# Kernel optimization log

Measured on AMD Instinct MI355X. Metric: run time of the kernel, lower is better.

The kernel has to match this reference:

```python
import jax, jax.numpy as jnp
import numpy as np

NP, NA, D, E, C, L = 100000, 50000, 128, 500000, 16, 2


def setup_inputs() -> dict:
    key = jax.random.key(0)
    ks = jax.random.split(key, 16)
    s = 1.0 / np.sqrt(D)
    ei_cites = jnp.stack([jax.random.randint(ks[2], (E,), 0, NP),
                          jax.random.randint(ks[3], (E,), 0, NP)])
    ei_writes = jnp.stack([jax.random.randint(ks[4], (E,), 0, NA),
                           jax.random.randint(ks[5], (E,), 0, NP)])
    ei_rev = jnp.stack([jax.random.randint(ks[6], (E,), 0, NP),
                        jax.random.randint(ks[7], (E,), 0, NA)])
    return {
        'x_paper': jax.random.normal(ks[0], (NP, D), jnp.float32),
        'x_author': jax.random.normal(ks[1], (NA, D), jnp.float32),
        'ei_cites': ei_cites, 'ei_writes': ei_writes, 'ei_rev': ei_rev,
        'Wl': jax.random.normal(ks[8], (L, 3, D, D), jnp.float32) * s,
        'Wr': jax.random.normal(ks[9], (L, 3, D, D), jnp.float32) * s,
        'bl': jnp.zeros((L, 3, D), jnp.float32),
        'lin_paper': jax.random.normal(ks[10], (D, D), jnp.float32) * s,
        'lin_author': jax.random.normal(ks[11], (D, D), jnp.float32) * s,
        'ln_scale': jnp.ones((L, 2, D), jnp.float32),
        'ln_bias': jnp.zeros((L, 2, D), jnp.float32),
        'Wh': jax.random.normal(ks[12], (D, C), jnp.float32) * s,
        'bh': jnp.zeros((C,), jnp.float32),
    }


def _sage(x_src, x_dst, ei, W_l, W_r, b, n_dst):
    # SAGEConv with mean aggregation: lin_l(mean_agg(x_src)) + lin_r(x_dst)
    msg = x_src[ei[0]]                                            # [E, D] gather
    ssum = jax.ops.segment_sum(msg, ei[1], num_segments=n_dst)    # [Ndst, D] scatter
    cnt = jax.ops.segment_sum(jnp.ones((ei.shape[1],), x_src.dtype), ei[1],
                              num_segments=n_dst)
    mean = ssum / jnp.maximum(cnt, 1.0)[:, None]
    return mean @ W_l.T + b + x_dst @ W_r.T


def _ln(x, g, b):
    m = jnp.mean(x, axis=-1, keepdims=True)
    v = jnp.mean(jnp.square(x - m), axis=-1, keepdims=True)
    return (x - m) * jax.lax.rsqrt(v + 1e-5) * g + b


def reference(x_paper, x_author, ei_cites, ei_writes, ei_rev,
              Wl, Wr, bl, lin_paper, lin_author, ln_scale, ln_bias, Wh, bh):
    x_p, x_a = x_paper, x_author
    n_p, n_a = x_p.shape[0], x_a.shape[0]
    for l in range(L):
        # HeteroConv: sum SAGEConv outputs per destination node type
        p_new = (_sage(x_p, x_p, ei_cites, Wl[l, 0], Wr[l, 0], bl[l, 0], n_p)
                 + _sage(x_a, x_p, ei_writes, Wl[l, 1], Wr[l, 1], bl[l, 1], n_p))
        a_new = _sage(x_p, x_a, ei_rev, Wl[l, 2], Wr[l, 2], bl[l, 2], n_a)
        if l < L - 1:  # per-type residual linear (use_linear)
            p_new = p_new + p_new @ lin_paper.T
            a_new = a_new + a_new @ lin_author.T
        x_p = jax.nn.relu(_ln(p_new, ln_scale[l, 0], ln_bias[l, 0]))
        x_a = jax.nn.relu(_ln(a_new, ln_scale[l, 1], ln_bias[l, 1]))
    # head on target node type ('paper')
    return x_p @ Wh + bh
```

## Files before the change

### kernel.cpp

```cpp
#include <hip/hip_runtime.h>
#include <math.h>

#define NPAPER 100000
#define NAUTH  50000
#define DIM    128
#define NEDGE  500000
#define NCLS   16
#define NTOT   (2*NPAPER + NAUTH)
#define NB     245
#define CHUNK_A 11776
#define NBLK_A  128
#define PBLK   ((NPAPER + 127) / 128)
#define ABLK   ((NAUTH  + 127) / 128)

typedef unsigned int   uint;
typedef unsigned short ushort;
typedef unsigned char  uchar;
using short8 = __attribute__((ext_vector_type(8))) short;
using f32x4  = __attribute__((ext_vector_type(4))) float;

__device__ __forceinline__ float b2f(uint u) {
    return __uint_as_float(u << 16);
}
__device__ __forceinline__ ushort f2b(float f) {
    uint x = __float_as_uint(f);
    return (ushort)((x + 0x7fffu + ((x >> 16) & 1u)) >> 16);
}

#define GLD_LDS16(srcp, ldsp) \
    __builtin_amdgcn_global_load_lds( \
        (const __attribute__((address_space(1))) void*)(srcp), \
        (__attribute__((address_space(3))) void*)(ldsp), 16, 0, 0)

__device__ __forceinline__ void prep_weights_body(int b, int tid,
    const float* __restrict__ Wl, const float* __restrict__ Wr,
    const float* __restrict__ bl,
    float* __restrict__ Bp, float* __restrict__ Ba,
    float* __restrict__ biasp, float* __restrict__ biasa)
{
    int t = b * 256 + tid;
    if (t < 2*384*128) {
        int l = t / (384*128); int rem = t - l*(384*128);
        int k = rem >> 7, j = rem & 127;
        float v;
        if (k < 128)      v = Wl[((l*3+0)*128 + j)*128 + k];
        else if (k < 256) v = Wl[((l*3+1)*128 + j)*128 + (k-128)];
        else              v = Wr[((l*3+0)*128 + j)*128 + (k-256)]
                            + Wr[((l*3+1)*128 + j)*128 + (k-256)];
        Bp[t] = v;
        return;
    }
    t -= 2*384*128;
    if (t < 2*256*128) {
        int l = t / (256*128); int rem = t - l*(256*128);
        int k = rem >> 7, j = rem & 127;
        Ba[t] = (k < 128) ? Wl[((l*3+2)*128 + j)*128 + k]
                          : Wr[((l*3+2)*128 + j)*128 + (k-128)];
        return;
    }
    t -= 2*256*128;
    if (t < 256) { int l=t>>7, j=t&127; biasp[t] = bl[(l*3+0)*128+j] + bl[(l*3+1)*128+j]; return; }
    t -= 256;
    if (t < 256) { int l=t>>7, j=t&127; biasa[t] = bl[(l*3+2)*128+j]; return; }
}

__device__ __forceinline__ size_t pack_off(int j, int k) {
    int kstep = k >> 6, ks = (k >> 5) & 1, g4 = (k >> 3) & 3, jj = k & 7;
    int f = j >> 4, l15 = j & 15;
    return (size_t)kstep*8192 + (size_t)(ks*512 + f*64 + g4*16 + l15)*8 + jj;
}

__device__ __forceinline__ void build_bt_body(int b, int tid,
    const float* __restrict__ Bp, const float* __restrict__ Ba,
    const float* __restrict__ linp, const float* __restrict__ lina,
    ushort* __restrict__ Btp, ushort* __restrict__ Bta)
{
    int t = b * 256 + tid;
    if (t < 2*128*384) {
        int l = t / (128*384); int rem = t - l*(128*384);
        int j = rem / 384, k = rem - j*384;
        const float* brow = Bp + (size_t)l*384*128 + (size_t)k*128;
        float v = brow[j];
        if (l == 0) {
            const float* lrow = linp + (size_t)j*128;
            float s = 0.f;
            #pragma unroll 8
            for (int m = 0; m < 128; m++) s += brow[m] * lrow[m];
            v += s;
        }
        Btp[(size_t)l*49152 + pack_off(j, k)] = f2b(v);
        return;
    }
    t -= 2*128*384;
    if (t < 2*128*256) {
        int l = t / (128*256); int rem = t - l*(128*256);
        int j = rem / 256, k = rem - j*256;
        const float* brow = Ba + (size_t)l*256*128 + (size_t)k*128;
        float v = brow[j];
        if (l == 0) {
            const float* lrow = lina + (size_t)j*128;
            float s = 0.f;
            #pragma unroll 8
            for (int m = 0; m < 128; m++) s += brow[m] * lrow[m];
            v += s;
        }
        Bta[(size_t)l*32768 + pack_off(j, k)] = f2b(v);
    }
}

__device__ __forceinline__ void fold_bias_body(int b, int tid,
    const float* __restrict__ biasp, const float* __restrict__ biasa,
    const float* __restrict__ linp, const float* __restrict__ lina,
    float* __restrict__ biasp2, float* __restrict__ biasa2)
{
    int t = b * 256 + tid;
    int isa = t >> 8; int r = t & 255;
    int l = r >> 7, j = r & 127;
    const float* bsrc = isa ? biasa : biasp;
    const float* lin  = isa ? lina  : linp;
    float v = bsrc[r];
    if (l == 0) {
        float s = 0.f;
        for (int k = 0; k < 128; k++) s += bsrc[k] * lin[j*128 + k];
        v += s;
    }
    (isa ? biasa2 : biasp2)[r] = v;
}

__device__ __forceinline__ void to_bf16_body(int b, int tid,
    const float* __restrict__ xp, const float* __restrict__ xa,
    ushort* __restrict__ yp, ushort* __restrict__ ya)
{
    int i = b * 256 + tid;
    const int n4p = NPAPER * DIM / 4;
    const float* x; ushort* y;
    if (i < n4p) { x = xp; y = yp; }
    else { x = xa; y = ya; i -= n4p; }
    float4 v = ((const float4*)x)[i];
    uint2 o;
    o.x = (uint)f2b(v.x) | ((uint)f2b(v.y) << 16);
    o.y = (uint)f2b(v.z) | ((uint)f2b(v.w) << 16);
    ((uint2*)y)[i] = o;
}

__device__ __forceinline__ int edge_g(const int* __restrict__ eiC,
                                      const int* __restrict__ eiW,
                                      const int* __restrict__ eiR, int i)
{
    int tpe = (i >= 2*NEDGE) ? 2 : ((i >= NEDGE) ? 1 : 0);
    int e = i - tpe*NEDGE;
    const int* ei = (tpe == 0) ? eiC : ((tpe == 1) ? eiW : eiR);
    int base = (tpe == 0) ? 0 : ((tpe == 1) ? NPAPER : 2*NPAPER);
    return base + ei[NEDGE + e];
}

#define PREPB 642
__global__ __launch_bounds__(256) void misc0(
    const int* __restrict__ eiC, const int* __restrict__ eiW,
    const int* __restrict__ eiR, int* __restrict__ bucketCount,
    const float* __restrict__ Wl, const float* __restrict__ Wr,
    const float* __restrict__ bl,
    float* __restrict__ Bp, float* __restrict__ Ba,
    float* __restrict__ biasp, float* __restrict__ biasa,
    const float* __restrict__ xpf, const float* __restrict__ xaf,
    ushort* __restrict__ xpb, ushort* __restrict__ xab)
{
    __shared__ int h[256];
    int b = blockIdx.x, t = threadIdx.x;
    if (b < NBLK_A) {
        h[t] = 0;
        __syncthreads();
        int start = b * CHUNK_A;
        int n = 3*NEDGE - start; if (n > CHUNK_A) n = CHUNK_A;
        for (int i = t; i < n; i += 256)
            atomicAdd(&h[edge_g(eiC, eiW, eiR, start + i) >> 10], 1);
        __syncthreads();
        if (h[t]) atomicAdd(&bucketCount[t], h[t]);
        return;
    }
    b -= NBLK_A;
    if (b < PREPB) {
        prep_weights_body(b, t, Wl, Wr, bl, Bp, Ba, biasp, biasa);
        return;
    }
    b -= PREPB;
    to_bf16_body(b, t, xpf, xaf, xpb, xab);
}

__global__ __launch_bounds__(256) void misc1(
    const int* __restrict__ bucketCount, int* __restrict__ bucketBase,
    int* __restrict__ stageCursor,
    const float* __restrict__ Bp, const float* __restrict__ Ba,
    const float* __restrict__ linp, const float* __restrict__ lina,
    ushort* __restrict__ Btp, ushort* __restrict__ Bta)
{
    __shared__ int lds[256];
    int b = blockIdx.x, t = threadIdx.x;
    if (b == 0) {
        int v = (t < NB) ? bucketCount[t] : 0;
        lds[t] = v;
        __syncthreads();
        for (int o = 1; o < 256; o <<= 1) {
            int x = (t >= o) ? lds[t - o] : 0;
            __syncthreads();
            lds[t] += x;
            __syncthreads();
        }
        int ex = lds[t] - v;
        if (t < NB) { bucketBase[t] = ex; stageCursor[t] = ex; }
        if (t == 0) bucketBase[NB] = 3*NEDGE;
        return;
    }
    build_bt_body(b - 1, t, Bp, Ba, linp, lina, Btp, Bta);
}

__global__ __launch_bounds__(256) void misc2(
    const float* __restrict__ biasp, const float* __restrict__ biasa,
    const float* __restrict__ linp, const float* __restrict__ lina,
    float* __restrict__ biasp2, float* __restrict__ biasa2,
    const int* __restrict__ eiC, const int* __restrict__ eiW,
    const int* __restrict__ eiR,
    int* __restrict__ stageCursor, uint2* __restrict__ stage)
{
    __shared__ uchar  bId [CHUNK_A];
    __shared__ ushort rnk [CHUNK_A];
    __shared__ ushort perm[CHUNK_A];
    __shared__ uchar  posB[CHUNK_A];
    __shared__ int lcnt[256];
    __shared__ int lpre[256];
    __shared__ int bbase[256];
    int blk = blockIdx.x, t = threadIdx.x;
    if (blk < 2) {
        fold_bias_body(blk, t, biasp, biasa, linp, lina, biasp2, biasa2);
        return;
    }
    int b = blk - 2;
    int start = b * CHUNK_A;
    int n = 3*NEDGE - start; if (n > CHUNK_A) n = CHUNK_A;
    lcnt[t] = 0;
    __syncthreads();
    for (int i = t; i < n; i += 256) {
        int bb = edge_g(eiC, eiW, eiR, start + i) >> 10;
        bId[i] = (uchar)bb;
        rnk[i] = (ushort)atomicAdd(&lcnt[bb], 1);
    }
    __syncthreads();
    lpre[t] = lcnt[t];
    __syncthreads();
    for (int o = 1; o < 256; o <<= 1) {
        int x = (t >= o) ? lpre[t - o] : 0;
        __syncthreads();
        lpre[t] += x;
        __syncthreads();
    }
    if (lcnt[t] > 0) bbase[t] = atomicAdd(&stageCursor[t], lcnt[t]);
    __syncthreads();
    for (int i = t; i < n; i += 256) {
        int bb = bId[i];
        int p = (lpre[bb] - lcnt[bb]) + rnk[i];
        perm[p] = (ushort)i;
        posB[p] = (uchar)bb;
    }
    __syncthreads();
    for (int p = t; p < n; p += 256) {
        int bb = posB[p];
        int i = start + perm[p];
        int tpe = (i >= 2*NEDGE) ? 2 : ((i >= NEDGE) ? 1 : 0);
        int e = i - tpe*NEDGE;
        const int* ei = (tpe == 0) ? eiC : ((tpe == 1) ? eiW : eiR);
        int base = (tpe == 0) ? 0 : ((tpe == 1) ? NPAPER : 2*NPAPER);
        uint2 o2;
        o2.x = (uint)(base + ei[NEDGE + e]);
        o2.y = (uint)ei[e];
        stage[bbase[bb] + (p - (lpre[bb] - lcnt[bb]))] = o2;
    }
}

__global__ __launch_bounds__(256) void csr_fillB(
    const uint2* __restrict__ stage, const int* __restrict__ bucketBase,
    int* __restrict__ rowAll, int* __restrict__ colAll)
{
    __shared__ int cnt[1024];
    __shared__ int part[256];
    int b = blockIdx.x;
    int t = threadIdx.x;
    int g0 = b << 10;
    int nn = NTOT - g0; if (nn > 1024) nn = 1024;
    int s = bucketBase[b], e = bucketBase[b+1];
    #pragma unroll
    for (int i = t; i < 1024; i += 256) cnt[i] = 0;
    __syncthreads();
    for (int i = s + t; i < e; i += 256) atomicAdd(&cnt[(int)stage[i].x - g0], 1);
    __syncthreads();
    int loc[4]; int ss = 0;
    #pragma unroll
    for (int j = 0; j < 4; j++) { loc[j] = cnt[t*4 + j]; ss += loc[j]; }
    part[t] = ss;
    __syncthreads();
    for (int o = 1; o < 256; o <<= 1) {
        int x = (t >= o) ? part[t - o] : 0;
        __syncthreads();
        part[t] += x;
        __syncthreads();
    }
    int run = (t > 0) ? part[t-1] : 0;
    #pragma unroll
    for (int j = 0; j < 4; j++) { int c = loc[j]; cnt[t*4 + j] = run; run += c; }
    __syncthreads();
    for (int i = t; i < nn; i += 256) rowAll[g0 + i] = s + cnt[i];
    if (b == NB-1 && t == 0) rowAll[NTOT] = 3*NEDGE;
    __syncthreads();
    for (int i = s + t; i < e; i += 256) {
        uint2 ed = stage[i];
        int slot = atomicAdd(&cnt[(int)ed.x - g0], 1);
        colAll[s + slot] = (int)ed.y;
    }
}

__device__ __forceinline__ void acc8(float* a, uint4 v) {
    a[0] += b2f(v.x & 0xffffu); a[1] += b2f(v.x >> 16);
    a[2] += b2f(v.y & 0xffffu); a[3] += b2f(v.y >> 16);
    a[4] += b2f(v.z & 0xffffu); a[5] += b2f(v.z >> 16);
    a[6] += b2f(v.w & 0xffffu); a[7] += b2f(v.w >> 16);
}

__global__ __launch_bounds__(256) void gather_seg(
    int g0, int g1,
    const ushort* __restrict__ xp, const ushort* __restrict__ xa,
    const int* __restrict__ rowAll, const int* __restrict__ colAll,
    ushort* __restrict__ aggC, ushort* __restrict__ aggW,
    ushort* __restrict__ aggR)
{
    int idx = blockIdx.x * 256 + threadIdx.x;
    int g = g0 + (idx >> 4);
    int lane = idx & 15;
    if (g >= g1) return;
    const ushort* xs; ushort* out; int node;
    if (g < NPAPER)        { node = g;            xs = xp; out = aggC; }
    else if (g < 2*NPAPER) { node = g - NPAPER;   xs = xa; out = aggW; }
    else                   { node = g - 2*NPAPER; xs = xp; out = aggR; }

    int s = rowAll[g], e = rowAll[g + 1];
    float a[8] = {0,0,0,0,0,0,0,0};
    float b[8] = {0,0,0,0,0,0,0,0};
    int j = s;
    #pragma unroll 1
    for (; j + 4 <= e; j += 4) {
        int s0 = colAll[j], s1 = colAll[j+1], s2 = colAll[j+2], s3 = colAll[j+3];
        uint4 v0 = *(const uint4*)(xs + (size_t)s0 * DIM + lane * 8);
        uint4 v1 = *(const uint4*)(xs + (size_t)s1 * DIM + lane * 8);
        uint4 v2 = *(const uint4*)(xs + (size_t)s2 * DIM + lane * 8);
        uint4 v3 = *(const uint4*)(xs + (size_t)s3 * DIM + lane * 8);
        acc8(a, v0);
        acc8(b, v1);
        acc8(a, v2);
        acc8(b, v3);
    }
    #pragma unroll 1
    for (; j < e; j++) {
        uint4 v0 = *(const uint4*)(xs + (size_t)colAll[j] * DIM + lane * 8);
        acc8(a, v0);
    }
    float inv = (e > s) ? 1.f / (float)(e - s) : 0.f;
    #pragma unroll
    for (int i = 0; i < 8; i++) a[i] = (a[i] + b[i]) * inv;
    uint4 o;
    o.x = (uint)f2b(a[0]) | ((uint)f2b(a[1]) << 16);
    o.y = (uint)f2b(a[2]) | ((uint)f2b(a[3]) << 16);
    o.z = (uint)f2b(a[4]) | ((uint)f2b(a[5]) << 16);
    o.w = (uint)f2b(a[6]) | ((uint)f2b(a[7]) << 16);
    *(uint4*)(out + (size_t)node * DIM + lane * 8) = o;
}

__global__ __launch_bounds__(256) void gemm_ln2(
    const ushort* __restrict__ aggC, const ushort* __restrict__ aggW,
    const ushort* __restrict__ aggR,
    const ushort* __restrict__ xp, const ushort* __restrict__ xa,
    const ushort* __restrict__ Btp, const ushort* __restrict__ Bta,
    const float* __restrict__ biasp, const float* __restrict__ biasa,
    const float* __restrict__ lns, const float* __restrict__ lnb,
    ushort* __restrict__ outp, ushort* __restrict__ outa, int pblk)
{
    __shared__ ushort As[8192];
    __shared__ ushort Bs[8192];

    bool isp = (int)blockIdx.x < pblk;
    int  bid = isp ? blockIdx.x : (blockIdx.x - pblk);
    int  N   = isp ? NPAPER : NAUTH;
    int  K   = isp ? 384 : 256;
    const ushort* A0 = isp ? aggC : aggR;
    const ushort* A1 = isp ? aggW : xa;
    const ushort* A2 = isp ? xp   : xa;
    const ushort* Bt = isp ? Btp  : Bta;
    const float* bias = isp ? biasp : biasa;
    const float* lng  = lns + (isp ? 0 : 128);
    const float* lnbb = lnb + (isp ? 0 : 128);
    ushort* out = isp ? outp : outa;

    int t    = threadIdx.x;
    int w    = t >> 6;
    int lane = t & 63;
    int row0 = bid * 128;
    int l15  = lane & 15;
    int g4   = lane >> 4;

    f32x4 acc0[8], acc1[8];
    #pragma unroll
    for (int f = 0; f < 8; f++) {
        acc0[f] = (f32x4){0.f, 0.f, 0.f, 0.f};
        acc1[f] = (f32x4){0.f, 0.f, 0.f, 0.f};
    }

    int nstep = K >> 6;
    for (int st = 0; st < nstep; st++) {
        int kk  = st << 6;
        int seg = kk >> 7, kl = kk & 127;
        const ushort* Ap = (seg == 0) ? A0 : ((seg == 1) ? A1 : A2);

        #pragma unroll
        for (int p = 0; p < 4; p++) {
            int q  = p*256 + t;
            int ks = q >> 9, rb = (q >> 6) & 7, l = q & 63;
            int row = row0 + rb*16 + (l & 15);
            row = (row < N) ? row : (N - 1);
            int k = kl + ks*32 + (l >> 4)*8;
            int qbase = p*256 + w*64;
            GLD_LDS16(Ap + (size_t)row*DIM + k, As + qbase*8);
        }
        #pragma unroll
        for (int p = 0; p < 4; p++) {
            int q = p*256 + t;
            int qbase = p*256 + w*64;
            GLD_LDS16(Bt + ((size_t)st*8192 + (size_t)q*8), Bs + qbase*8);
        }
        __syncthreads();

        #pragma unroll
        for (int ks = 0; ks < 2; ks++) {
            short8 a0 = *(const short8*)(&As[((ks*8 + w*2 + 0)*64 + lane)*8]);
            short8 a1 = *(const short8*)(&As[((ks*8 + w*2 + 1)*64 + lane)*8]);
            #pragma unroll
            for (int f = 0; f < 8; f++) {
                short8 bv = *(const short8*)(&Bs[((ks*8 + f)*64 + lane)*8]);
                acc0[f] = __builtin_amdgcn_mfma_f32_16x16x32_bf16(a0, bv, acc0[f], 0, 0, 0);
                acc1[f] = __builtin_amdgcn_mfma_f32_16x16x32_bf16(a1, bv, acc1[f], 0, 0, 0);
            }
        }
        __syncthreads();
    }

    float bv[8], gv[8], bbv[8];
    #pragma unroll
    for (int f = 0; f < 8; f++) {
        bv[f]  = bias[f*16 + l15];
        gv[f]  = lng [f*16 + l15];
        bbv[f] = lnbb[f*16 + l15];
    }
    #pragma unroll
    for (int r2 = 0; r2 < 2; r2++) {
        #pragma unroll
        for (int i = 0; i < 4; i++) {
            int grow = row0 + w*32 + r2*16 + g4*4 + i;
            float vv[8];
            float s = 0.f, sq = 0.f;
            #pragma unroll
            for (int f = 0; f < 8; f++) {
                float av = r2 ? acc1[f][i] : acc0[f][i];
                vv[f] = av + bv[f];
                s  += vv[f];
                sq += vv[f] * vv[f];
            }
            s += __shfl_xor(s, 1);  sq += __shfl_xor(sq, 1);
            s += __shfl_xor(s, 2);  sq += __shfl_xor(sq, 2);
            s += __shfl_xor(s, 4);  sq += __shfl_xor(sq, 4);
            s += __shfl_xor(s, 8);  sq += __shfl_xor(sq, 8);
            float m   = s * (1.f/128.f);
            float var = sq * (1.f/128.f) - m*m;
            float rr  = rsqrtf(var + 1e-5f);
            if (grow < N) {
                #pragma unroll
                for (int f = 0; f < 8; f++) {
                    float y = (vv[f] - m) * rr * gv[f] + bbv[f];
                    y = fmaxf(y, 0.f);
                    out[(size_t)grow*DIM + f*16 + l15] = f2b(y);
                }
            }
        }
    }
}

__global__ __launch_bounds__(256) void head_kernel(
    const ushort* __restrict__ xp, const float* __restrict__ Wh,
    const float* __restrict__ bh, float* __restrict__ out)
{
    __shared__ float Xs[16*128];
    __shared__ float Ws[128*16];
    int t = threadIdx.x;
    int row0 = blockIdx.x * 16;
    for (int i = t; i < 2048; i += 256) Ws[i] = Wh[i];
    {
        int r = t >> 4, k8 = (t & 15) * 8;
        int gr = row0 + r;
        if (gr < NPAPER) {
            uint4 v = *(const uint4*)(xp + (size_t)gr*DIM + k8);
            const ushort* pv = (const ushort*)&v;
            #pragma unroll
            for (int i = 0; i < 8; i++) Xs[r*128 + k8 + i] = b2f(pv[i]);
        } else {
            #pragma unroll
            for (int i = 0; i < 8; i++) Xs[r*128 + k8 + i] = 0.f;
        }
    }
    __syncthreads();
    int r = t >> 4, c = t & 15;
    float acc = bh[c];
    #pragma unroll 16
    for (int k = 0; k < 128; k++) acc += Xs[r*128 + k] * Ws[k*16 + c];
    int gr = row0 + r;
    if (gr < NPAPER) out[(size_t)gr*NCLS + c] = acc;
}

extern "C" void kernel_launch(void* const* d_in, const int* in_sizes, int n_in,
                              void* d_out, int out_size, void* d_ws, size_t ws_size,
                              hipStream_t stream)
{
    const float* x_paper  = (const float*)d_in[0];
    const float* x_author = (const float*)d_in[1];
    const int*   ei_cites = (const int*)d_in[2];
    const int*   ei_writes= (const int*)d_in[3];
    const int*   ei_rev   = (const int*)d_in[4];
    const float* Wl       = (const float*)d_in[5];
    const float* Wr       = (const float*)d_in[6];
    const float* bl       = (const float*)d_in[7];
    const float* linp     = (const float*)d_in[8];
    const float* lina     = (const float*)d_in[9];
    const float* ln_s     = (const float*)d_in[10];
    const float* ln_b     = (const float*)d_in[11];
    const float* Wh       = (const float*)d_in[12];
    const float* bh       = (const float*)d_in[13];
    float* out = (float*)d_out;

    float* ws = (float*)d_ws;
    size_t off = 0;
    float* Bp     = ws + off; off += 2*384*128;
    float* Ba     = ws + off; off += 2*256*128;
    float* biasp  = ws + off; off += 2*128;
    float* biasa  = ws + off; off += 2*128;
    float* biasp2 = ws + off; off += 2*128;
    float* biasa2 = ws + off; off += 2*128;

    ushort* uws = (ushort*)(ws + off);
    size_t uoff = 0;
    ushort* xpb0 = uws + uoff; uoff += (size_t)NPAPER * DIM;
    ushort* xab0 = uws + uoff; uoff += (size_t)NAUTH  * DIM;
    ushort* xpb1 = uws + uoff; uoff += (size_t)NPAPER * DIM;
    ushort* xab1 = uws + uoff; uoff += (size_t)NAUTH  * DIM;
    ushort* aggC = uws + uoff; uoff += (size_t)NPAPER * DIM;
    ushort* aggW = uws + uoff; uoff += (size_t)NPAPER * DIM;
    ushort* aggR = uws + uoff; uoff += (size_t)NAUTH  * DIM;
    ushort* Btp  = uws + uoff; uoff += 2*49152;
    ushort* Bta  = uws + uoff; uoff += 2*32768;
    if (uoff & 3) uoff += 4 - (uoff & 3);

    uint2* stage = (uint2*)(uws + uoff);
    int* iws = (int*)(stage + 3*NEDGE);
    size_t ioff = 0;
    int* rowAll      = iws + ioff; ioff += NTOT + 1;
    int* colAll      = iws + ioff; ioff += 3*NEDGE;
    int* bucketCount = iws + ioff; ioff += 256;
    int* bucketBase  = iws + ioff; ioff += 256 + 1;
    int* stageCursor = iws + ioff; ioff += 256;

    const int TOBF = (NPAPER + NAUTH) * DIM / 4 / 256;

    hipMemsetAsync(bucketCount, 0, 256*4, stream);
    misc0<<<NBLK_A + PREPB + TOBF, 256, 0, stream>>>(
        ei_cites, ei_writes, ei_rev, bucketCount,
        Wl, Wr, bl, Bp, Ba, biasp, biasa,
        x_paper, x_author, xpb0, xab0);
    misc1<<<1 + 640, 256, 0, stream>>>(
        bucketCount, bucketBase, stageCursor, Bp, Ba, linp, lina, Btp, Bta);
    misc2<<<2 + NBLK_A, 256, 0, stream>>>(
        biasp, biasa, linp, lina, biasp2, biasa2,
        ei_cites, ei_writes, ei_rev, stageCursor, stage);
    csr_fillB<<<NB, 256, 0, stream>>>(stage, bucketBase, rowAll, colAll);

    gather_seg<<<(size_t)NTOT*16/256, 256, 0, stream>>>(
        0, NTOT, xpb0, xab0, rowAll, colAll, aggC, aggW, aggR);
    gemm_ln2<<<PBLK + ABLK, 256, 0, stream>>>(
        aggC, aggW, aggR, xpb0, xab0,
        Btp, Bta, biasp2, biasa2, ln_s, ln_b,
        xpb1, xab1, PBLK);

    gather_seg<<<(size_t)2*NPAPER*16/256, 256, 0, stream>>>(
        0, 2*NPAPER, xpb1, xab1, rowAll, colAll, aggC, aggW, aggR);
    gemm_ln2<<<PBLK, 256, 0, stream>>>(
        aggC, aggW, aggR, xpb1, xab1,
        Btp + 49152, Bta + 32768, biasp2 + 128, biasa2 + 128,
        ln_s + 256, ln_b + 256,
        xpb0, xab0, PBLK);

    head_kernel<<<(NPAPER + 15)/16, 256, 0, stream>>>(xpb0, Wh, bh, out);
}
```

Measured before the change: 309.1 us.

## Merge misc1/misc2 with redundant per-block scan, widen gather to one wave per row

The bucket prefix scan is now recomputed inside each scatter block and each CSR-fill block, which lets misc1 and misc2 merge into one launch. Staging offsets now come from the recomputed base plus a zeroed emit cursor. The gather kernel switches from 16 lanes doing 16-byte loads per destination row to 64 lanes doing 4-byte loads. The aim is to cut one launch and dependency and to change memory-level parallelism in the gather, at the cost of redundant scans and more, narrower memory requests.

```diff
diff --git a/kernel.cpp b/kernel.cpp
--- a/kernel.cpp
+++ b/kernel.cpp
@@ -187,41 +187,30 @@
     to_bf16_body(b, t, xpf, xaf, xpb, xab);
 }
 
+#define BTB 640
 __global__ __launch_bounds__(256) void misc1(
-    const int* __restrict__ bucketCount, int* __restrict__ bucketBase,
-    int* __restrict__ stageCursor,
-    const float* __restrict__ Bp, const float* __restrict__ Ba,
-    const float* __restrict__ linp, const float* __restrict__ lina,
-    ushort* __restrict__ Btp, ushort* __restrict__ Bta)
-{
-    __shared__ int lds[256];
-    int b = blockIdx.x, t = threadIdx.x;
-    if (b == 0) {
-        int v = (t < NB) ? bucketCount[t] : 0;
-        lds[t] = v;
-        __syncthreads();
-        for (int o = 1; o < 256; o <<= 1) {
-            int x = (t >= o) ? lds[t - o] : 0;
-            __syncthreads();
-            lds[t] += x;
-            __syncthreads();
-        }
-        int ex = lds[t] - v;
-        if (t < NB) { bucketBase[t] = ex; stageCursor[t] = ex; }
-        if (t == 0) bucketBase[NB] = 3*NEDGE;
-        return;
-    }
-    build_bt_body(b - 1, t, Bp, Ba, linp, lina, Btp, Bta);
-}
-
-__global__ __launch_bounds__(256) void misc2(
     const float* __restrict__ biasp, const float* __restrict__ biasa,
     const float* __restrict__ linp, const float* __restrict__ lina,
     float* __restrict__ biasp2, float* __restrict__ biasa2,
+    const float* __restrict__ Bp, const float* __restrict__ Ba,
+    ushort* __restrict__ Btp, ushort* __restrict__ Bta,
     const int* __restrict__ eiC, const int* __restrict__ eiW,
     const int* __restrict__ eiR,
-    int* __restrict__ stageCursor, uint2* __restrict__ stage)
-{
+    const int* __restrict__ bucketCount, int* __restrict__ emitCursor,
+    uint2* __restrict__ stage)
+{
+    int blk = blockIdx.x, t = threadIdx.x;
+    if (blk < 2) {
+        fold_bias_body(blk, t, biasp, biasa, linp, lina, biasp2, biasa2);
+        return;
+    }
+    blk -= 2;
+    if (blk < BTB) {
+        build_bt_body(blk, t, Bp, Ba, linp, lina, Btp, Bta);
+        return;
+    }
+    int b = blk - BTB;
+
     __shared__ uchar  bId [CHUNK_A];
     __shared__ ushort rnk [CHUNK_A];
     __shared__ ushort perm[CHUNK_A];
@@ -229,12 +218,24 @@
     __shared__ int lcnt[256];
     __shared__ int lpre[256];
     __shared__ int bbase[256];
-    int blk = blockIdx.x, t = threadIdx.x;
-    if (blk < 2) {
-        fold_bias_body(blk, t, biasp, biasa, linp, lina, biasp2, biasa2);
-        return;
-    }
-    int b = blk - 2;
+    __shared__ int bbs[256];
+
+    {
+        int v = (t < NB) ? bucketCount[t] : 0;
+        bbs[t] = v;
+        __syncthreads();
+        for (int o = 1; o < 256; o <<= 1) {
+            int x = (t >= o) ? bbs[t - o] : 0;
+            __syncthreads();
+            bbs[t] += x;
+            __syncthreads();
+        }
+        int inc = bbs[t];
+        __syncthreads();
+        bbs[t] = inc - ((t < NB) ? bucketCount[t] : 0);
+        __syncthreads();
+    }
+
     int start = b * CHUNK_A;
     int n = 3*NEDGE - start; if (n > CHUNK_A) n = CHUNK_A;
     lcnt[t] = 0;
@@ -253,7 +254,7 @@
         lpre[t] += x;
         __syncthreads();
     }
-    if (lcnt[t] > 0) bbase[t] = atomicAdd(&stageCursor[t], lcnt[t]);
+    if (lcnt[t] > 0) bbase[t] = bbs[t] + atomicAdd(&emitCursor[t], lcnt[t]);
     __syncthreads();
     for (int i = t; i < n; i += 256) {
         int bb = bId[i];
@@ -277,16 +278,35 @@
 }
 
 __global__ __launch_bounds__(256) void csr_fillB(
-    const uint2* __restrict__ stage, const int* __restrict__ bucketBase,
+    const uint2* __restrict__ stage, const int* __restrict__ bucketCount,
     int* __restrict__ rowAll, int* __restrict__ colAll)
 {
     __shared__ int cnt[1024];
     __shared__ int part[256];
+    __shared__ int bbs[256];
     int b = blockIdx.x;
     int t = threadIdx.x;
+
+    {
+        int v = (t < NB) ? bucketCount[t] : 0;
+        bbs[t] = v;
+        __syncthreads();
+        for (int o = 1; o < 256; o <<= 1) {
+            int x = (t >= o) ? bbs[t - o] : 0;
+            __syncthreads();
+            bbs[t] += x;
+            __syncthreads();
+        }
+        int inc = bbs[t];
+        __syncthreads();
+        bbs[t] = inc - ((t < NB) ? bucketCount[t] : 0);
+        __syncthreads();
+    }
     int g0 = b << 10;
     int nn = NTOT - g0; if (nn > 1024) nn = 1024;
-    int s = bucketBase[b], e = bucketBase[b+1];
+    int s = bbs[b];
+    int e = s + bucketCount[b];
+
     #pragma unroll
     for (int i = t; i < 1024; i += 256) cnt[i] = 0;
     __syncthreads();
@@ -315,13 +335,6 @@
         int slot = atomicAdd(&cnt[(int)ed.x - g0], 1);
         colAll[s + slot] = (int)ed.y;
     }
-}
-
-__device__ __forceinline__ void acc8(float* a, uint4 v) {
-    a[0] += b2f(v.x & 0xffffu); a[1] += b2f(v.x >> 16);
-    a[2] += b2f(v.y & 0xffffu); a[3] += b2f(v.y >> 16);
-    a[4] += b2f(v.z & 0xffffu); a[5] += b2f(v.z >> 16);
-    a[6] += b2f(v.w & 0xffffu); a[7] += b2f(v.w >> 16);
 }
 
 __global__ __launch_bounds__(256) void gather_seg(
@@ -331,9 +344,8 @@
     ushort* __restrict__ aggC, ushort* __restrict__ aggW,
     ushort* __restrict__ aggR)
 {
-    int idx = blockIdx.x * 256 + threadIdx.x;
-    int g = g0 + (idx >> 4);
-    int lane = idx & 15;
+    int g = g0 + ((blockIdx.x * 256 + threadIdx.x) >> 6);
+    int lane = threadIdx.x & 63;
     if (g >= g1) return;
     const ushort* xs; ushort* out; int node;
     if (g < NPAPER)        { node = g;            xs = xp; out = aggC; }
@@ -341,35 +353,30 @@
     else                   { node = g - 2*NPAPER; xs = xp; out = aggR; }
 
     int s = rowAll[g], e = rowAll[g + 1];
-    float a[8] = {0,0,0,0,0,0,0,0};
-    float b[8] = {0,0,0,0,0,0,0,0};
+    float a0 = 0.f, a1 = 0.f, b0 = 0.f, b1 = 0.f;
     int j = s;
     #pragma unroll 1
     for (; j + 4 <= e; j += 4) {
         int s0 = colAll[j], s1 = colAll[j+1], s2 = colAll[j+2], s3 = colAll[j+3];
-        uint4 v0 = *(const uint4*)(xs + (size_t)s0 * DIM + lane * 8);
-        uint4 v1 = *(const uint4*)(xs + (size_t)s1 * DIM + lane * 8);
-        uint4 v2 = *(const uint4*)(xs + (size_t)s2 * DIM + lane * 8);
-        uint4 v3 = *(const uint4*)(xs + (size_t)s3 * DIM + lane * 8);
-        acc8(a, v0);
-        acc8(b, v1);
-        acc8(a, v2);
-        acc8(b, v3);
+        uint v0 = *(const uint*)(xs + (size_t)s0 * DIM + lane * 2);
+        uint v1 = *(const uint*)(xs + (size_t)s1 * DIM + lane * 2);
+        uint v2 = *(const uint*)(xs + (size_t)s2 * DIM + lane * 2);
+        uint v3 = *(const uint*)(xs + (size_t)s3 * DIM + lane * 2);
+        a0 += b2f(v0 & 0xffffu); a1 += b2f(v0 >> 16);
+        b0 += b2f(v1 & 0xffffu); b1 += b2f(v1 >> 16);
+        a0 += b2f(v2 & 0xffffu); a1 += b2f(v2 >> 16);
+        b0 += b2f(v3 & 0xffffu); b1 += b2f(v3 >> 16);
     }
     #pragma unroll 1
     for (; j < e; j++) {
-        uint4 v0 = *(const uint4*)(xs + (size_t)colAll[j] * DIM + lane * 8);
-        acc8(a, v0);
+        uint v = *(const uint*)(xs + (size_t)colAll[j] * DIM + lane * 2);
+        a0 += b2f(v & 0xffffu); a1 += b2f(v >> 16);
     }
     float inv = (e > s) ? 1.f / (float)(e - s) : 0.f;
-    #pragma unroll
-    for (int i = 0; i < 8; i++) a[i] = (a[i] + b[i]) * inv;
-    uint4 o;
-    o.x = (uint)f2b(a[0]) | ((uint)f2b(a[1]) << 16);
-    o.y = (uint)f2b(a[2]) | ((uint)f2b(a[3]) << 16);
-    o.z = (uint)f2b(a[4]) | ((uint)f2b(a[5]) << 16);
-    o.w = (uint)f2b(a[6]) | ((uint)f2b(a[7]) << 16);
-    *(uint4*)(out + (size_t)node * DIM + lane * 8) = o;
+    a0 = (a0 + b0) * inv;
+    a1 = (a1 + b1) * inv;
+    uint o = (uint)f2b(a0) | ((uint)f2b(a1) << 16);
+    *(uint*)(out + (size_t)node * DIM + lane * 2) = o;
 }
 
 __global__ __launch_bounds__(256) void gemm_ln2(
@@ -568,31 +575,30 @@
     int* rowAll      = iws + ioff; ioff += NTOT + 1;
     int* colAll      = iws + ioff; ioff += 3*NEDGE;
     int* bucketCount = iws + ioff; ioff += 256;
-    int* bucketBase  = iws + ioff; ioff += 256 + 1;
-    int* stageCursor = iws + ioff; ioff += 256;
+    int* emitCursor  = iws + ioff; ioff += 256;
 
     const int TOBF = (NPAPER + NAUTH) * DIM / 4 / 256;
 
-    hipMemsetAsync(bucketCount, 0, 256*4, stream);
+    hipMemsetAsync(bucketCount, 0, 512*4, stream);
     misc0<<<NBLK_A + PREPB + TOBF, 256, 0, stream>>>(
         ei_cites, ei_writes, ei_rev, bucketCount,
         Wl, Wr, bl, Bp, Ba, biasp, biasa,
         x_paper, x_author, xpb0, xab0);
-    misc1<<<1 + 640, 256, 0, stream>>>(
-        bucketCount, bucketBase, stageCursor, Bp, Ba, linp, lina, Btp, Bta);
-    misc2<<<2 + NBLK_A, 256, 0, stream>>>(
+    misc1<<<2 + BTB + NBLK_A, 256, 0, stream>>>(
         biasp, biasa, linp, lina, biasp2, biasa2,
-        ei_cites, ei_writes, ei_rev, stageCursor, stage);
-    csr_fillB<<<NB, 256, 0, stream>>>(stage, bucketBase, rowAll, colAll);
-
-    gather_seg<<<(size_t)NTOT*16/256, 256, 0, stream>>>(
+        Bp, Ba, Btp, Bta,
+        ei_cites, ei_writes, ei_rev,
+        bucketCount, emitCursor, stage);
+    csr_fillB<<<NB, 256, 0, stream>>>(stage, bucketCount, rowAll, colAll);
+
+    gather_seg<<<(NTOT + 3)/4, 256, 0, stream>>>(
         0, NTOT, xpb0, xab0, rowAll, colAll, aggC, aggW, aggR);
     gemm_ln2<<<PBLK + ABLK, 256, 0, stream>>>(
         aggC, aggW, aggR, xpb0, xab0,
         Btp, Bta, biasp2, biasa2, ln_s, ln_b,
         xpb1, xab1, PBLK);
 
-    gather_seg<<<(size_t)2*NPAPER*16/256, 256, 0, stream>>>(
+    gather_seg<<<(2*NPAPER + 3)/4, 256, 0, stream>>>(
         0, 2*NPAPER, xpb1, xab1, rowAll, colAll, aggC, aggW, aggR);
     gemm_ln2<<<PBLK, 256, 0, stream>>>(
         aggC, aggW, aggR, xpb1, xab1,
```

Measured after the change: 365.6 us. +18.3%, slower.
